# Performance work log

Measured on AMD Instinct MI355X. Metric: run time of the kernel, lower is better.

The kernel has to match this reference:

```python
import jax, jax.numpy as jnp
import numpy as np

N = 100000   # nodes
E = 1000000  # edges
IN = 100     # input feature dim
H = 4        # heads
D = 32       # hidden per head (H*D = 128)
C = 47       # classes
EPS = 1e-5
SLOPE = 0.2  # DGL GATv2 leaky_relu negative slope


def setup_inputs() -> dict:
    key = jax.random.key(0)
    ks = jax.random.split(key, 32)
    lin = lambda k, i, o: (jax.random.normal(k, (i, o), jnp.float32) / np.float32(np.sqrt(i)))
    inp = {}
    inp['x'] = jax.random.normal(ks[0], (N, IN), jnp.float32)
    inp['src'] = jax.random.randint(ks[1], (E,), 0, N, jnp.int32)
    inp['dst'] = jnp.sort(jax.random.randint(ks[2], (E,), 0, N, jnp.int32))
    # layer 0: IN -> H*D, Linear residual (IN != H*D)
    inp['Wsrc0'] = lin(ks[3], IN, H * D); inp['bsrc0'] = jnp.zeros(H * D, jnp.float32)
    inp['Wdst0'] = lin(ks[4], IN, H * D); inp['bdst0'] = jnp.zeros(H * D, jnp.float32)
    inp['attn0'] = lin(ks[5], H, D)
    inp['Wres0'] = lin(ks[6], IN, H * D); inp['bres0'] = jnp.zeros(H * D, jnp.float32)
    # layer 1: H*D -> H*D, Identity residual (128 == 128)
    inp['Wsrc1'] = lin(ks[7], H * D, H * D); inp['bsrc1'] = jnp.zeros(H * D, jnp.float32)
    inp['Wdst1'] = lin(ks[8], H * D, H * D); inp['bdst1'] = jnp.zeros(H * D, jnp.float32)
    inp['attn1'] = lin(ks[9], H, D)
    # layer 2: H*D -> H*C, Linear residual (128 != 188)
    inp['Wsrc2'] = lin(ks[10], H * D, H * C); inp['bsrc2'] = jnp.zeros(H * C, jnp.float32)
    inp['Wdst2'] = lin(ks[11], H * D, H * C); inp['bdst2'] = jnp.zeros(H * C, jnp.float32)
    inp['attn2'] = lin(ks[12], H, C)
    inp['Wres2'] = lin(ks[13], H * D, H * C); inp['bres2'] = jnp.zeros(H * C, jnp.float32)
    # BatchNorm1d params (training-mode batch stats)
    inp['g0'] = jnp.ones(H * D, jnp.float32); inp['be0'] = jnp.zeros(H * D, jnp.float32)
    inp['g1'] = jnp.ones(H * D, jnp.float32); inp['be1'] = jnp.zeros(H * D, jnp.float32)
    return inp


def _gatv2(h, src, dst, Ws, bs, Wd, bd, attn, resval):
    """One GATv2Conv on a full block (src feats == dst feats == h)."""
    Hh, Dd = attn.shape
    fs = (h @ Ws + bs).reshape(-1, Hh, Dd)   # [N,H,D] src projection
    fd = (h @ Wd + bd).reshape(-1, Hh, Dd)   # [N,H,D] dst projection
    e = jax.nn.leaky_relu(fs[src] + fd[dst], SLOPE)         # [E,H,D]
    logits = jnp.einsum('ehd,hd->eh', e, attn)              # [E,H]
    m = jax.ops.segment_max(logits, dst, num_segments=N)    # per-dst max
    ex = jnp.exp(logits - m[dst])
    s = jax.ops.segment_sum(ex, dst, num_segments=N)
    alpha = ex / s[dst]                                      # edge softmax
    out = jax.ops.segment_sum(alpha[:, :, None] * fs[src], dst, num_segments=N)
    return out + resval                                      # [N,H,D]


def _bn(x, g, b):
    mu = x.mean(0)
    v = x.var(0)  # biased, as torch BN training mode
    return g * (x - mu) / jnp.sqrt(v + EPS) + b


def reference(x, src, dst,
              Wsrc0, bsrc0, Wdst0, bdst0, attn0, Wres0, bres0,
              Wsrc1, bsrc1, Wdst1, bdst1, attn1,
              Wsrc2, bsrc2, Wdst2, bdst2, attn2, Wres2, bres2,
              g0, be0, g1, be1):
    # layer 0: conv(+relu activation) -> flatten -> BN -> relu (dropout = eval identity)
    res0 = (x @ Wres0 + bres0).reshape(N, H, D)
    h = jax.nn.relu(_gatv2(x, src, dst, Wsrc0, bsrc0, Wdst0, bdst0, attn0, res0))
    h = jax.nn.relu(_bn(h.reshape(N, H * D), g0, be0))
    # layer 1: Identity residual
    res1 = h.reshape(N, H, D)
    h = jax.nn.relu(_gatv2(h, src, dst, Wsrc1, bsrc1, Wdst1, bdst1, attn1, res1))
    h = jax.nn.relu(_bn(h.reshape(N, H * D), g1, be1))
    # layer 2: no activation; mean over heads; log_softmax
    res2 = (h @ Wres2 + bres2).reshape(N, H, C)
    h = _gatv2(h, src, dst, Wsrc2, bsrc2, Wdst2, bdst2, attn2, res2)
    h = h.mean(1)                                # [N,C]
    return jax.nn.log_softmax(h, axis=-1)
```

## Files before the change

kernel.cpp:

```cpp
#include <hip/hip_runtime.h>
#include <hip/hip_bf16.h>

#define Nn 100000
#define Ee 1000000
#define INF_ 100
#define Hh 4
#define Dd 32
#define HD 128
#define Cc 47
#define HC 188
#define HCP 192
#define EPSV 1e-5f
#define SLOPE 0.2f
#define NBLK ((Nn + 255) / 256)

typedef __hip_bfloat16 bf16;
typedef __attribute__((ext_vector_type(8))) short short8;
typedef __attribute__((ext_vector_type(4))) float f32x4;
typedef __attribute__((ext_vector_type(2))) float f32x2;

__device__ __forceinline__ float tof(bf16 v) { return __bfloat162float(v); }
__device__ __forceinline__ float b2f(unsigned short u) {
    return __uint_as_float((unsigned)u << 16);
}
__device__ __forceinline__ float b2flo(unsigned u) {
    return __uint_as_float(u << 16);
}
__device__ __forceinline__ float b2fhi(unsigned u) {
    return __uint_as_float(u & 0xFFFF0000u);
}
__device__ __forceinline__ float ldb(const bf16* p) {
    return b2f(*(const unsigned short*)p);
}
__device__ __forceinline__ unsigned short f2u(float v) {
    bf16 t = __float2bfloat16(v);
    return *(unsigned short*)&t;
}
__device__ __forceinline__ f32x2 pk2(float x, float y) {
    f32x2 r; r.x = x; r.y = y; return r;
}
__device__ __forceinline__ f32x2 pabs2(f32x2 v) {
    return __builtin_elementwise_max(v, -v);
}
__device__ __forceinline__ f32x2 pfma2(f32x2 a, f32x2 b, f32x2 c) {
    return __builtin_elementwise_fma(a, b, c);
}

template <int C>
__device__ __forceinline__ float dppadd(float v) {
    int m = __builtin_amdgcn_update_dpp(0, __float_as_int(v), C, 0xF, 0xF, false);
    return v + __int_as_float(m);
}
template <int C>
__device__ __forceinline__ float dppmax(float v) {
    int m = __builtin_amdgcn_update_dpp(0, __float_as_int(v), C, 0xF, 0xF, false);
    return fmaxf(v, __int_as_float(m));
}
__device__ __forceinline__ float sum16(float p) {
    p = dppadd<0xB1>(p);
    p = dppadd<0x4E>(p);
    p = dppadd<0x124>(p);
    p = dppadd<0x128>(p);
    return p;
}
__device__ __forceinline__ float max16(float p) {
    p = dppmax<0xB1>(p); p = dppmax<0x4E>(p);
    p = dppmax<0x124>(p); p = dppmax<0x128>(p);
    return p;
}

#define L2E 1.4426950408889634f
#define LN2 0.6931471805599453f

__global__ void detect_dtype(const unsigned* __restrict__ x, int* __restrict__ flag) {
    if (blockIdx.x == 0 && threadIdx.x == 0) {
        int good = 0;
        for (int i = 0; i < 256; ++i) {
            unsigned lo = x[i] & 0xFFFFu;
            float v = __uint_as_float(lo << 16);
            float a = fabsf(v);
            if (a > 1e-4f && a < 10.f) good++;
        }
        *flag = (good >= 128) ? 1 : 0;
    }
}

__device__ __forceinline__ float ld_any(const void* p, int i, int isbf) {
    return isbf ? tof(((const bf16*)p)[i]) : ((const float*)p)[i];
}

__global__ void cvt_x(const void* __restrict__ in, bf16* __restrict__ out,
                      const int* __restrict__ flag) {
    int i = blockIdx.x * blockDim.x + threadIdx.x;
    if (i >= Nn * 128) return;
    int row = i >> 7, col = i & 127;
    float v = (col < INF_) ? ld_any(in, row * INF_ + col, *flag) : 0.f;
    out[i] = __float2bfloat16(v);
}

#define NSP 15
struct CvtTab { const void* src[NSP]; int off[NSP + 1]; };

__global__ void cvt_params(CvtTab t, bf16* __restrict__ out, int total,
                           const int* __restrict__ flag) {
    int i = blockIdx.x * blockDim.x + threadIdx.x;
    if (i >= total) return;
    int isbf = *flag;
    int seg = 0;
    while (i >= t.off[seg + 1]) seg++;
    out[i] = __float2bfloat16(ld_any(t.src[seg], i - t.off[seg], isbf));
}

#define WROWS 1280
struct PrepTab { const void* src[8]; int row0[8]; int K[8]; int M[8]; int MP[8]; };

__global__ void prep_all(PrepTab t, bf16* __restrict__ wtb, const int* __restrict__ flag) {
    int i = blockIdx.x * blockDim.x + threadIdx.x;
    if (i >= WROWS * 128) return;
    int row = i >> 7, k = i & 127;
    int isbf = *flag;
    float v = 0.f;
#pragma unroll
    for (int q = 0; q < 8; ++q) {
        if (row >= t.row0[q] && row < t.row0[q] + t.MP[q]) {
            int m = row - t.row0[q];
            if (m < t.M[q] && k < t.K[q])
                v = ld_any(t.src[q], k * t.M[q] + m, isbf);
        }
    }
    wtb[i] = __float2bfloat16(v);
}

__global__ void zero_u32(unsigned* __restrict__ p, int n) {
    int i = blockIdx.x * blockDim.x + threadIdx.x;
    if (i < n) p[i] = 0u;
}

__global__ void src_scale_ptr(const int* __restrict__ src, const int* __restrict__ dst,
                              unsigned* __restrict__ w384, unsigned* __restrict__ w256,
                              int* __restrict__ ptr) {
    int i = blockIdx.x * blockDim.x + threadIdx.x;
    if (i < Ee) {
        unsigned s = (unsigned)src[i];
        w384[i] = s * 384u;
        w256[i] = s << 8;
    }
    if (i <= Nn) {
        if (i == Nn) { ptr[Nn] = Ee; return; }
        int lo = 0, hi = Ee;
        while (lo < hi) {
            int mid = (lo + hi) >> 1;
            if (dst[mid] < i) lo = mid + 1; else hi = mid;
        }
        ptr[i] = lo;
    }
}

__global__ void deg_hist_blk(const int* __restrict__ ptr, int* __restrict__ cnt) {
    __shared__ int lh[256];
    int t = threadIdx.x;
    lh[t] = 0;
    __syncthreads();
    int n = blockIdx.x * 256 + t;
    if (n < Nn) {
        int dg = ptr[n + 1] - ptr[n]; if (dg > 255) dg = 255;
        atomicAdd(&lh[dg], 1);
    }
    __syncthreads();
    cnt[t * NBLK + blockIdx.x] = lh[t];
}

__global__ void deg_totals(const int* __restrict__ cnt, int* __restrict__ totals) {
    int wave = threadIdx.x >> 6, lane = threadIdx.x & 63;
    int bin = blockIdx.x * 4 + wave;
    int s = 0;
    for (int k = lane; k < NBLK; k += 64) s += cnt[bin * NBLK + k];
#pragma unroll
    for (int o = 1; o < 64; o <<= 1) s += __shfl_xor(s, o);
    if (lane == 0) totals[bin] = s;
}

__global__ void deg_bases(const int* __restrict__ cnt, const int* __restrict__ totals,
                          int* __restrict__ base) {
    int wave = threadIdx.x >> 6, lane = threadIdx.x & 63;
    int bin = blockIdx.x * 4 + wave;
    int bb = 0;
    for (int b = bin + 1 + lane; b < 256; b += 64) bb += totals[b];
#pragma unroll
    for (int o = 1; o < 64; o <<= 1) bb += __shfl_xor(bb, o);
    int run = bb;
    for (int k0 = 0; k0 < NBLK; k0 += 64) {
        int k = k0 + lane;
        int c = (k < NBLK) ? cnt[bin * NBLK + k] : 0;
        int p = c;
#pragma unroll
        for (int o = 1; o < 64; o <<= 1) {
            int t = __shfl_up(p, o);
            if (lane >= o) p += t;
        }
        if (k < NBLK) base[bin * NBLK + k] = run + (p - c);
        run += __shfl(p, 63);
    }
}

__global__ void deg_scatter_blk(const int* __restrict__ ptr, const int* __restrict__ base,
                                int* __restrict__ perm) {
    __shared__ int lh[256];
    int t = threadIdx.x;
    lh[t] = 0;
    __syncthreads();
    int n = blockIdx.x * 256 + t;
    if (n < Nn) {
        int dg = ptr[n + 1] - ptr[n]; if (dg > 255) dg = 255;
        int loc = atomicAdd(&lh[dg], 1);
        perm[base[dg * NBLK + blockIdx.x] + loc] = n;
    }
}

template <int MP, int NOUT, int CS, bool ABN, bool PACK, int OSTR, int NY>
__global__ __launch_bounds__(256, 4) void gemm_big(
    const bf16* __restrict__ A, const bf16* __restrict__ Wt,
    const bf16* __restrict__ b0, const bf16* __restrict__ b1,
    const bf16* __restrict__ b2,
    bf16* __restrict__ o0, bf16* __restrict__ o1, bf16* __restrict__ o2,
    int MR, const float* __restrict__ bnp) {
    __shared__ __align__(16) bf16 Al[64 * 136];
    const int row0 = blockIdx.x * 64;
    const int tid = threadIdx.x;
#pragma unroll
    for (int j = 0; j < 4; ++j) {
        int idx = tid + j * 256;
        int r = idx >> 4, kk = (idx & 15) * 8;
        int4 val = {0, 0, 0, 0};
        if (row0 + r < Nn) {
            val = *(const int4*)&A[(size_t)(row0 + r) * 128 + kk];
            if (ABN) {
                short8 av = *(short8*)&val;
                bf16 tmp[8];
#pragma unroll
                for (int u = 0; u < 8; ++u) {
                    float v = b2f((unsigned short)av[u]);
                    v = fmaxf(fmaf(v, bnp[kk + u], bnp[128 + kk + u]), 0.f);
                    tmp[u] = __float2bfloat16(v);
                }
                val = *(int4*)tmp;
            }
        }
        *(int4*)&Al[r * 136 + kk] = val;
    }
    __syncthreads();
    const int wave = tid >> 6, lane = tid & 63;
    const int n16 = lane & 15, quad = lane >> 4;
    const bf16* ap = Al + n16 * 136 + quad * 8;
#pragma unroll
    for (int ny = 0; ny < NY; ++ny) {
        const int colbase = ny * (64 * CS) + wave * (16 * CS);
        f32x4 acc[4][CS];
#pragma unroll
        for (int rt = 0; rt < 4; ++rt)
#pragma unroll
            for (int c = 0; c < CS; ++c) acc[rt][c] = (f32x4){0.f, 0.f, 0.f, 0.f};
        const bf16* wb[CS];
#pragma unroll
        for (int c = 0; c < CS; ++c)
            wb[c] = Wt + (size_t)(colbase + c * 16 + n16) * 128 + quad * 8;
#pragma unroll
        for (int ks = 0; ks < 4; ++ks) {
            short8 bf[CS];
#pragma unroll
            for (int c = 0; c < CS; ++c) bf[c] = *(const short8*)(wb[c] + ks * 32);
#pragma unroll
            for (int rt = 0; rt < 4; ++rt) {
                short8 af = *(const short8*)(ap + rt * 16 * 136 + ks * 32);
#pragma unroll
                for (int c = 0; c < CS; ++c)
                    acc[rt][c] = __builtin_amdgcn_mfma_f32_16x16x32_bf16(af, bf[c], acc[rt][c], 0, 0, 0);
            }
        }
#pragma unroll
        for (int c = 0; c < CS; ++c) {
            int col = colbase + c * 16 + n16;
            int oi = col / MP, lc = col - oi * MP;
            if (oi >= NOUT || lc >= MR) continue;
            const bf16* bp = (oi == 0) ? b0 : (oi == 1) ? b1 : b2;
            bf16* o = (oi == 0) ? o0 : (oi == 1) ? o1 : o2;
            float bb = tof(bp[lc]);
            int st;
            if (PACK) {
                int hh = lc / 47, cc = lc - hh * 47;
                int jj = cc & 15, kk2 = cc >> 4;
                int l = hh * 16 + jj;
                st = (kk2 < 2) ? (2 * l + kk2) : (128 + l);
            } else {
                st = lc;
            }
#pragma unroll
            for (int rt = 0; rt < 4; ++rt) {
#pragma unroll
                for (int i = 0; i < 4; ++i) {
                    int row = row0 + rt * 16 + quad * 4 + i;
                    if (row < Nn)
                        o[(size_t)row * OSTR + st] = __float2bfloat16(acc[rt][c][i] + bb);
                }
            }
        }
    }
}

template <bool RESBN>
__global__ __launch_bounds__(256) void gat_fused_128(
    const bf16* __restrict__ fs, const bf16* __restrict__ fd,
    const unsigned* __restrict__ srcW, const int* __restrict__ ptr,
    const int* __restrict__ perm,
    const bf16* __restrict__ attn, const bf16* __restrict__ resb,
    const float* __restrict__ bnp, bf16* __restrict__ hout) {
    const int wave = threadIdx.x >> 6, lane = threadIdx.x & 63;
    const int di = blockIdx.x * 4 + wave;
    if (di >= Nn) return;
    const int d = perm[di];
    const int c0 = lane * 2;
    const unsigned c0b = (unsigned)c0 * 2u;
    ushort2 aq = *(const ushort2*)&attn[c0];
    float a0 = b2f(aq.x) * L2E, a1 = b2f(aq.y) * L2E;
    const f32x2 Av = pk2(0.6f * a0, 0.6f * a1);
    const f32x2 Bv = pk2(0.4f * a0, 0.4f * a1);
    ushort2 dq = *(const ushort2*)&fd[(size_t)d * HD + c0];
    const f32x2 fdv = pk2(b2f(dq.x), b2f(dq.y));
    const char* fsb = (const char*)fs;
    float l = 0.f;
    f32x2 Ov = pk2(0.f, 0.f);
    int e = ptr[d];
    const int e1 = ptr[d + 1];
    for (; e < e1 && (e & 3); ++e) {
        unsigned v = srcW[e] + c0b;
        ushort2 fq = *(const ushort2*)(fsb + v);
        f32x2 f = pk2(b2f(fq.x), b2f(fq.y));
        f32x2 x = f + fdv;
        f32x2 t = pfma2(pabs2(x), Bv, x * Av);
        float p = sum16(t.x + t.y);
        float pe = __builtin_amdgcn_exp2f(p);
        l += pe;
        Ov = pfma2(pk2(pe, pe), f, Ov);
    }
    for (; e + 3 < e1; e += 4) {
        uint4 sw = *(const uint4*)&srcW[e];
        unsigned vA = sw.x + c0b, vB = sw.y + c0b;
        unsigned vC = sw.z + c0b, vD = sw.w + c0b;
        ushort2 qA = *(const ushort2*)(fsb + vA);
        ushort2 qB = *(const ushort2*)(fsb + vB);
        ushort2 qC = *(const ushort2*)(fsb + vC);
        ushort2 qD = *(const ushort2*)(fsb + vD);
        f32x2 fA = pk2(b2f(qA.x), b2f(qA.y));
        f32x2 fB = pk2(b2f(qB.x), b2f(qB.y));
        f32x2 fC = pk2(b2f(qC.x), b2f(qC.y));
        f32x2 fD = pk2(b2f(qD.x), b2f(qD.y));
        f32x2 xA = fA + fdv, xB = fB + fdv, xC = fC + fdv, xD = fD + fdv;
        f32x2 tA = pfma2(pabs2(xA), Bv, xA * Av);
        f32x2 tB = pfma2(pabs2(xB), Bv, xB * Av);
        f32x2 tC = pfma2(pabs2(xC), Bv, xC * Av);
        f32x2 tD = pfma2(pabs2(xD), Bv, xD * Av);
        float pA = tA.x + tA.y, pB = tB.x + tB.y;
        float pC = tC.x + tC.y, pD = tD.x + tD.y;
        pA = sum16(pA); pB = sum16(pB); pC = sum16(pC); pD = sum16(pD);
        float eA = __builtin_amdgcn_exp2f(pA), eB = __builtin_amdgcn_exp2f(pB);
        float eC = __builtin_amdgcn_exp2f(pC), eD = __builtin_amdgcn_exp2f(pD);
        l += (eA + eB) + (eC + eD);
        Ov = pfma2(pk2(eA, eA), fA, Ov);
        Ov = pfma2(pk2(eB, eB), fB, Ov);
        Ov = pfma2(pk2(eC, eC), fC, Ov);
        Ov = pfma2(pk2(eD, eD), fD, Ov);
    }
    for (; e < e1; ++e) {
        unsigned v = srcW[e] + c0b;
        ushort2 fq = *(const ushort2*)(fsb + v);
        f32x2 f = pk2(b2f(fq.x), b2f(fq.y));
        f32x2 x = f + fdv;
        f32x2 t = pfma2(pabs2(x), Bv, x * Av);
        float p = sum16(t.x + t.y);
        float pe = __builtin_amdgcn_exp2f(p);
        l += pe;
        Ov = pfma2(pk2(pe, pe), f, Ov);
    }
    float inv = l > 0.f ? 1.f / l : 0.f;
    ushort2 rq = *(const ushort2*)&resb[(size_t)d * HD + c0];
    float r0 = b2f(rq.x), r1 = b2f(rq.y);
    if (RESBN) {
        r0 = fmaxf(fmaf(r0, bnp[c0], bnp[HD + c0]), 0.f);
        r1 = fmaxf(fmaf(r1, bnp[c0 + 1], bnp[HD + c0 + 1]), 0.f);
    }
    float v0 = fmaxf(fmaf(Ov.x, inv, r0), 0.f);
    float v1 = fmaxf(fmaf(Ov.y, inv, r1), 0.f);
    ushort2 ov; ov.x = f2u(v0); ov.y = f2u(v1);
    *(ushort2*)&hout[(size_t)d * HD + c0] = ov;
}

__global__ __launch_bounds__(256) void gat_fused_188(
    const bf16* __restrict__ fs, const bf16* __restrict__ fd,
    const unsigned* __restrict__ srcW, const int* __restrict__ ptr,
    const int* __restrict__ perm,
    const bf16* __restrict__ attn, const bf16* __restrict__ rs,
    void* __restrict__ out, const int* __restrict__ flag) {
    const int wave = threadIdx.x >> 6, lane = threadIdx.x & 63;
    const int di = blockIdx.x * 4 + wave;
    if (di >= Nn) return;
    const int d = perm[di];
    const int h = lane >> 4, j = lane & 15;
    const unsigned cbA = (unsigned)lane * 4u;
    const unsigned cbB = 256u + (unsigned)lane * 2u;
    const int ca = h * Cc + j;
    const bool has2 = (j < 15);
    float a0 = ldb(&attn[ca]) * L2E;
    float a1 = ldb(&attn[ca + 16]) * L2E;
    float a2 = has2 ? ldb(&attn[ca + 32]) * L2E : 0.f;
    const f32x2 Av = pk2(0.6f * a0, 0.6f * a1);
    const f32x2 Bv = pk2(0.4f * a0, 0.4f * a1);
    const float A2 = 0.6f * a2, B2 = 0.4f * a2;
    const char* fdb = (const char*)fd;
    const size_t drow = (size_t)d * 384u;
    unsigned dqa = *(const unsigned*)(fdb + drow + cbA);
    unsigned short dqb = *(const unsigned short*)(fdb + drow + cbB);
    const f32x2 fdv = pk2(b2flo(dqa), b2fhi(dqa));
    const float fd2 = b2f(dqb);
    const char* fsb = (const char*)fs;
    float l = 0.f, O2 = 0.f;
    f32x2 Ov = pk2(0.f, 0.f);
    int e = ptr[d];
    const int e1 = ptr[d + 1];
    for (; e < e1 && (e & 3); ++e) {
        unsigned b = srcW[e];
        unsigned q = *(const unsigned*)(fsb + b + cbA);
        unsigned short u = *(const unsigned short*)(fsb + b + cbB);
        f32x2 f = pk2(b2flo(q), b2fhi(q)); float g = b2f(u);
        f32x2 x = f + fdv;
        float y = g + fd2;
        f32x2 t = pfma2(pabs2(x), Bv, x * Av);
        float p = fmaf(y, A2, fmaf(fabsf(y), B2, t.x + t.y));
        p = sum16(p);
        float pe = __builtin_amdgcn_exp2f(p);
        l += pe;
        Ov = pfma2(pk2(pe, pe), f, Ov); O2 = fmaf(pe, g, O2);
    }
    for (; e + 3 < e1; e += 4) {
        uint4 sw = *(const uint4*)&srcW[e];
        unsigned bA = sw.x, bB = sw.y, bC = sw.z, bD = sw.w;
        unsigned qA = *(const unsigned*)(fsb + bA + cbA);
        unsigned qB = *(const unsigned*)(fsb + bB + cbA);
        unsigned qC = *(const unsigned*)(fsb + bC + cbA);
        unsigned qD = *(const unsigned*)(fsb + bD + cbA);
        unsigned short uA = *(const unsigned short*)(fsb + bA + cbB);
        unsigned short uB = *(const unsigned short*)(fsb + bB + cbB);
        unsigned short uC = *(const unsigned short*)(fsb + bC + cbB);
        unsigned short uD = *(const unsigned short*)(fsb + bD + cbB);
        f32x2 fA = pk2(b2flo(qA), b2fhi(qA)); float gA = b2f(uA);
        f32x2 fB = pk2(b2flo(qB), b2fhi(qB)); float gB = b2f(uB);
        f32x2 fC = pk2(b2flo(qC), b2fhi(qC)); float gC = b2f(uC);
        f32x2 fD = pk2(b2flo(qD), b2fhi(qD)); float gD = b2f(uD);
        f32x2 xA = fA + fdv, xB = fB + fdv, xC = fC + fdv, xD = fD + fdv;
        float yA = gA + fd2, yB = gB + fd2, yC = gC + fd2, yD = gD + fd2;
        f32x2 tA = pfma2(pabs2(xA), Bv, xA * Av);
        f32x2 tB = pfma2(pabs2(xB), Bv, xB * Av);
        f32x2 tC = pfma2(pabs2(xC), Bv, xC * Av);
        f32x2 tD = pfma2(pabs2(xD), Bv, xD * Av);
        float pA = fmaf(yA, A2, fmaf(fabsf(yA), B2, tA.x + tA.y));
        float pB = fmaf(yB, A2, fmaf(fabsf(yB), B2, tB.x + tB.y));
        float pC = fmaf(yC, A2, fmaf(fabsf(yC), B2, tC.x + tC.y));
        float pD = fmaf(yD, A2, fmaf(fabsf(yD), B2, tD.x + tD.y));
        pA = sum16(pA); pB = sum16(pB); pC = sum16(pC); pD = sum16(pD);
        float eA = __builtin_amdgcn_exp2f(pA), eB = __builtin_amdgcn_exp2f(pB);
        float eC = __builtin_amdgcn_exp2f(pC), eD = __builtin_amdgcn_exp2f(pD);
        l += (eA + eB) + (eC + eD);
        Ov = pfma2(pk2(eA, eA), fA, Ov); O2 = fmaf(eA, gA, O2);
        Ov = pfma2(pk2(eB, eB), fB, Ov); O2 = fmaf(eB, gB, O2);
        Ov = pfma2(pk2(eC, eC), fC, Ov); O2 = fmaf(eC, gC, O2);
        Ov = pfma2(pk2(eD, eD), fD, Ov); O2 = fmaf(eD, gD, O2);
    }
    for (; e < e1; ++e) {
        unsigned b = srcW[e];
        unsigned q = *(const unsigned*)(fsb + b + cbA);
        unsigned short u = *(const unsigned short*)(fsb + b + cbB);
        f32x2 f = pk2(b2flo(q), b2fhi(q)); float g = b2f(u);
        f32x2 x = f + fdv;
        float y = g + fd2;
        f32x2 t = pfma2(pabs2(x), Bv, x * Av);
        float p = fmaf(y, A2, fmaf(fabsf(y), B2, t.x + t.y));
        p = sum16(p);
        float pe = __builtin_amdgcn_exp2f(p);
        l += pe;
        Ov = pfma2(pk2(pe, pe), f, Ov); O2 = fmaf(pe, g, O2);
    }
    float inv = l > 0.f ? 1.f / l : 0.f;
    const char* rb_ = (const char*)rs;
    unsigned rqa = *(const unsigned*)(rb_ + drow + cbA);
    unsigned short rqb = *(const unsigned short*)(rb_ + drow + cbB);
    float v0 = fmaf(Ov.x, inv, b2flo(rqa));
    float v1 = fmaf(Ov.y, inv, b2fhi(rqa));
    float v2 = has2 ? fmaf(O2, inv, b2f(rqb)) : 0.f;
    v0 += __shfl_xor(v0, 16); v0 += __shfl_xor(v0, 32); v0 *= 0.25f;
    v1 += __shfl_xor(v1, 16); v1 += __shfl_xor(v1, 32); v1 *= 0.25f;
    v2 += __shfl_xor(v2, 16); v2 += __shfl_xor(v2, 32); v2 *= 0.25f;
    float mx = fmaxf(v0, v1);
    if (has2) mx = fmaxf(mx, v2);
    mx = max16(mx);
    float sm = __expf(v0 - mx) + __expf(v1 - mx) + (has2 ? __expf(v2 - mx) : 0.f);
    sm = sum16(sm);
    if (h == 0) {
        float ls = mx + __log2f(sm) * LN2;
        if (*flag) {
            bf16* o = (bf16*)out + (size_t)d * Cc;
            o[j] = __float2bfloat16(v0 - ls);
            o[j + 16] = __float2bfloat16(v1 - ls);
            if (has2) o[j + 32] = __float2bfloat16(v2 - ls);
        } else {
            float* o = (float*)out + (size_t)d * Cc;
            o[j] = v0 - ls;
            o[j + 16] = v1 - ls;
            if (has2) o[j + 32] = v2 - ls;
        }
    }
}

__global__ void col_stats(const bf16* __restrict__ in, float* __restrict__ sums) {
    int c = threadIdx.x;
    int r0 = blockIdx.x * 256;
    int r1 = r0 + 256; if (r1 > Nn) r1 = Nn;
    float s = 0.f, s2 = 0.f;
    for (int r = r0; r < r1; ++r) {
        float v = ldb(&in[(size_t)r * HD + c]);
        s += v; s2 += v * v;
    }
    atomicAdd(&sums[c], s);
    atomicAdd(&sums[HD + c], s2);
}

__global__ void bn_finalize(const float* __restrict__ sums, const bf16* __restrict__ g,
                            const bf16* __restrict__ be, float* __restrict__ ss) {
    int c = threadIdx.x;
    float mu = sums[c] * (1.f / Nn);
    float var = sums[HD + c] * (1.f / Nn) - mu * mu;
    float sc = tof(g[c]) * rsqrtf(var + EPSV);
    ss[c] = sc;
    ss[HD + c] = tof(be[c]) - mu * sc;
}

extern "C" void kernel_launch(void* const* d_in, const int* in_sizes, int n_in,
                              void* d_out, int out_size, void* d_ws, size_t ws_size,
                              hipStream_t stream) {
    (void)in_sizes; (void)n_in; (void)out_size; (void)ws_size;
    const void* x = d_in[0];
    const int* src = (const int*)d_in[1];
    const int* dst = (const int*)d_in[2];

    char* ws = (char*)d_ws;
    size_t off = 0;
    auto alloc = [&](size_t bytes) {
        void* p = ws + off;
        off += (bytes + 255) & ~(size_t)255;
        return p;
    };
    bf16* xb = (bf16*)alloc((size_t)Nn * 128 * 2);
    bf16* rb = (bf16*)alloc((size_t)Nn * HD * 2);
    bf16* rs = xb;
    bf16* fs = (bf16*)alloc((size_t)Nn * HCP * 2);
    bf16* fd = (bf16*)alloc((size_t)Nn * HCP * 2);
    bf16* hbA = (bf16*)alloc((size_t)Nn * HD * 2);
    bf16* hbB = (bf16*)alloc((size_t)Nn * HD * 2);
    int* ptr = (int*)alloc((Nn + 1) * 4);
    bf16* wtb = (bf16*)alloc((size_t)WROWS * 128 * 2);
    float* bns = (float*)alloc(2 * HD * 4);
    float* bnss0 = (float*)alloc(2 * HD * 4);
    float* bnss1 = (float*)alloc(2 * HD * 4);
    bf16* pb = (bf16*)alloc(4096 * 2);
    int* flag = (int*)alloc(256);
    unsigned* w384 = (unsigned*)alloc((size_t)Ee * 4);
    unsigned* w256 = (unsigned*)alloc((size_t)Ee * 4);
    int* cnt = (int*)alloc((size_t)256 * NBLK * 4);
    int* cbase = (int*)alloc((size_t)256 * NBLK * 4);
    int* totals = (int*)alloc(256 * 4);
    int* perm = (int*)alloc((size_t)Nn * 4);

    static const int spIdx[NSP] = {4, 6, 7, 9, 11, 13, 14, 16, 18, 19, 21, 22, 23, 24, 25};
    static const int spSz[NSP]  = {HD, HD, HD, HD, HD, HD, HD, HC, HC, HC, HC, HD, HD, HD, HD};
    CvtTab tab;
    int tot = 0;
    for (int i = 0; i < NSP; ++i) { tab.src[i] = d_in[spIdx[i]]; tab.off[i] = tot; tot += spSz[i]; }
    tab.off[NSP] = tot;
    const bf16 *bsrc0 = pb + tab.off[0], *bdst0 = pb + tab.off[1], *attn0 = pb + tab.off[2],
               *bres0 = pb + tab.off[3], *bsrc1 = pb + tab.off[4], *bdst1 = pb + tab.off[5],
               *attn1 = pb + tab.off[6], *bsrc2 = pb + tab.off[7], *bdst2 = pb + tab.off[8],
               *attn2 = pb + tab.off[9], *bres2 = pb + tab.off[10],
               *g0 = pb + tab.off[11], *be0 = pb + tab.off[12],
               *g1 = pb + tab.off[13], *be1 = pb + tab.off[14];

    PrepTab pt;
    static const int wIdx[8] = {3, 5, 8, 10, 12, 15, 17, 20};
    static const int wK[8]   = {INF_, INF_, INF_, HD, HD, HD, HD, HD};
    static const int wM[8]   = {HD, HD, HD, HD, HD, HC, HC, HC};
    static const int wMP[8]  = {128, 128, 128, 128, 128, 192, 192, 192};
    static const int wR0[8]  = {0, 128, 256, 384, 512, 640, 832, 1024};
    for (int i = 0; i < 8; ++i) {
        pt.src[i] = d_in[wIdx[i]]; pt.row0[i] = wR0[i];
        pt.K[i] = wK[i]; pt.M[i] = wM[i]; pt.MP[i] = wMP[i];
    }

    detect_dtype<<<1, 64, 0, stream>>>((const unsigned*)x, flag);
    cvt_x<<<(Nn * 128 + 255) / 256, 256, 0, stream>>>(x, xb, flag);
    cvt_params<<<(tot + 255) / 256, 256, 0, stream>>>(tab, pb, tot, flag);
    prep_all<<<(WROWS * 128 + 255) / 256, 256, 0, stream>>>(pt, wtb, flag);
    src_scale_ptr<<<(Ee + 255) / 256, 256, 0, stream>>>(src, dst, w384, w256, ptr);
    deg_hist_blk<<<NBLK, 256, 0, stream>>>(ptr, cnt);
    deg_totals<<<64, 256, 0, stream>>>(cnt, totals);
    deg_bases<<<64, 256, 0, stream>>>(cnt, totals, cbase);
    deg_scatter_blk<<<NBLK, 256, 0, stream>>>(ptr, cbase, perm);

    const int fusedGrid = (Nn + 3) / 4;
    const int statsGrid = NBLK;
    const int rowBlk = (Nn + 63) / 64;

    gemm_big<128, 3, 3, false, false, HD, 2><<<rowBlk, 256, 0, stream>>>(
        xb, wtb, bsrc0, bdst0, bres0, fs, fd, rb, HD, nullptr);
    gat_fused_128<false><<<fusedGrid, 256, 0, stream>>>(fs, fd, w256, ptr, perm,
                                                        attn0, rb, nullptr, hbA);
    zero_u32<<<1, 256, 0, stream>>>((unsigned*)bns, 2 * HD);
    col_stats<<<statsGrid, 128, 0, stream>>>(hbA, bns);
    bn_finalize<<<1, HD, 0, stream>>>(bns, g0, be0, bnss0);

    gemm_big<128, 2, 2, true, false, HD, 2><<<rowBlk, 256, 0, stream>>>(
        hbA, wtb + (size_t)384 * 128, bsrc1, bdst1, nullptr, fs, fd, nullptr, HD, bnss0);
    gat_fused_128<true><<<fusedGrid, 256, 0, stream>>>(fs, fd, w256, ptr, perm,
                                                       attn1, hbA, bnss0, hbB);
    zero_u32<<<1, 256, 0, stream>>>((unsigned*)bns, 2 * HD);
    col_stats<<<statsGrid, 128, 0, stream>>>(hbB, bns);
    bn_finalize<<<1, HD, 0, stream>>>(bns, g1, be1, bnss1);

    gemm_big<192, 3, 3, true, true, HCP, 3><<<rowBlk, 256, 0, stream>>>(
        hbB, wtb + (size_t)640 * 128, bsrc2, bdst2, bres2, fs, fd, rs, HC, bnss1);
    gat_fused_188<<<fusedGrid, 256, 0, stream>>>(fs, fd, w384, ptr, perm, attn2, rs,
                                                 d_out, flag);
}
```

Measured before the change: 704.8 us.

## Merge setup kernels, split GEMM column tiles across grid y, widen GAT blocks

Merges the parameter conversion into the weight-prep kernel and moves the BN-stat zeroing into src_scale_ptr, using separate stat buffers per layer so two zero_u32 launches go away. The GEMM column loop (NY) becomes a second grid dimension, giving more independent blocks at the cost of each block reloading its A tile into LDS. The GAT kernels go from 4 to 8 waves per block. Launch count drops and parallelism rises, but A-tile loads and LDS traffic are duplicated across the grid-y blocks.

Measured after the change: 698.3 us. About the same (-0.9%).

```diff
diff --git a/kernel.cpp b/kernel.cpp
--- a/kernel.cpp
+++ b/kernel.cpp
@@ -98,53 +98,47 @@
     out[i] = __float2bfloat16(v);
 }
 
+#define WROWS 1280
 #define NSP 15
+struct PrepTab { const void* src[8]; int row0[8]; int K[8]; int M[8]; int MP[8]; };
 struct CvtTab { const void* src[NSP]; int off[NSP + 1]; };
 
-__global__ void cvt_params(CvtTab t, bf16* __restrict__ out, int total,
-                           const int* __restrict__ flag) {
+__global__ void prep_all(PrepTab t, CvtTab ct, bf16* __restrict__ wtb,
+                         bf16* __restrict__ pb, int total,
+                         const int* __restrict__ flag) {
     int i = blockIdx.x * blockDim.x + threadIdx.x;
-    if (i >= total) return;
     int isbf = *flag;
-    int seg = 0;
-    while (i >= t.off[seg + 1]) seg++;
-    out[i] = __float2bfloat16(ld_any(t.src[seg], i - t.off[seg], isbf));
-}
-
-#define WROWS 1280
-struct PrepTab { const void* src[8]; int row0[8]; int K[8]; int M[8]; int MP[8]; };
-
-__global__ void prep_all(PrepTab t, bf16* __restrict__ wtb, const int* __restrict__ flag) {
-    int i = blockIdx.x * blockDim.x + threadIdx.x;
-    if (i >= WROWS * 128) return;
-    int row = i >> 7, k = i & 127;
-    int isbf = *flag;
-    float v = 0.f;
-#pragma unroll
-    for (int q = 0; q < 8; ++q) {
-        if (row >= t.row0[q] && row < t.row0[q] + t.MP[q]) {
-            int m = row - t.row0[q];
-            if (m < t.M[q] && k < t.K[q])
-                v = ld_any(t.src[q], k * t.M[q] + m, isbf);
-        }
-    }
-    wtb[i] = __float2bfloat16(v);
-}
-
-__global__ void zero_u32(unsigned* __restrict__ p, int n) {
-    int i = blockIdx.x * blockDim.x + threadIdx.x;
-    if (i < n) p[i] = 0u;
+    if (i < WROWS * 128) {
+        int row = i >> 7, k = i & 127;
+        float v = 0.f;
+#pragma unroll
+        for (int q = 0; q < 8; ++q) {
+            if (row >= t.row0[q] && row < t.row0[q] + t.MP[q]) {
+                int m = row - t.row0[q];
+                if (m < t.M[q] && k < t.K[q])
+                    v = ld_any(t.src[q], k * t.M[q] + m, isbf);
+            }
+        }
+        wtb[i] = __float2bfloat16(v);
+    }
+    if (i < total) {
+        int seg = 0;
+        while (i >= ct.off[seg + 1]) seg++;
+        pb[i] = __float2bfloat16(ld_any(ct.src[seg], i - ct.off[seg], isbf));
+    }
 }
 
 __global__ void src_scale_ptr(const int* __restrict__ src, const int* __restrict__ dst,
                               unsigned* __restrict__ w384, unsigned* __restrict__ w256,
-                              int* __restrict__ ptr) {
+                              int* __restrict__ ptr,
+                              float* __restrict__ z0, float* __restrict__ z1) {
     int i = blockIdx.x * blockDim.x + threadIdx.x;
     if (i < Ee) {
         unsigned s = (unsigned)src[i];
         w384[i] = s * 384u;
         w256[i] = s << 8;
     }
+    if (i < 2 * HD) { z0[i] = 0.f; z1[i] = 0.f; }
     if (i <= Nn) {
         if (i == Nn) { ptr[Nn] = Ee; return; }
         int lo = 0, hi = Ee;
@@ -217,7 +211,7 @@
     }
 }
 
-template <int MP, int NOUT, int CS, bool ABN, bool PACK, int OSTR, int NY>
+template <int MP, int NOUT, int CS, bool ABN, bool PACK, int OSTR>
 __global__ __launch_bounds__(256, 4) void gemm_big(
     const bf16* __restrict__ A, const bf16* __restrict__ Wt,
     const bf16* __restrict__ b0, const bf16* __restrict__ b1,
@@ -251,71 +245,68 @@
     __syncthreads();
     const int wave = tid >> 6, lane = tid & 63;
     const int n16 = lane & 15, quad = lane >> 4;
+    const int colbase = blockIdx.y * (64 * CS) + wave * (16 * CS);
+    f32x4 acc[4][CS];
+#pragma unroll
+    for (int rt = 0; rt < 4; ++rt)
+#pragma unroll
+        for (int c = 0; c < CS; ++c) acc[rt][c] = (f32x4){0.f, 0.f, 0.f, 0.f};
+    const bf16* wb[CS];
+#pragma unroll
+    for (int c = 0; c < CS; ++c)
+        wb[c] = Wt + (size_t)(colbase + c * 16 + n16) * 128 + quad * 8;
     const bf16* ap = Al + n16 * 136 + quad * 8;
 #pragma unroll
-    for (int ny = 0; ny < NY; ++ny) {
-        const int colbase = ny * (64 * CS) + wave * (16 * CS);
-        f32x4 acc[4][CS];
-#pragma unroll
-        for (int rt = 0; rt < 4; ++rt)
-#pragma unroll
-            for (int c = 0; c < CS; ++c) acc[rt][c] = (f32x4){0.f, 0.f, 0.f, 0.f};
-        const bf16* wb[CS];
-#pragma unroll
-        for (int c = 0; c < CS; ++c)
-            wb[c] = Wt + (size_t)(colbase + c * 16 + n16) * 128 + quad * 8;
-#pragma unroll
-        for (int ks = 0; ks < 4; ++ks) {
-            short8 bf[CS];
-#pragma unroll
-            for (int c = 0; c < CS; ++c) bf[c] = *(const short8*)(wb[c] + ks * 32);
-#pragma unroll
-            for (int rt = 0; rt < 4; ++rt) {
-                short8 af = *(const short8*)(ap + rt * 16 * 136 + ks * 32);
-#pragma unroll
-                for (int c = 0; c < CS; ++c)
-                    acc[rt][c] = __builtin_amdgcn_mfma_f32_16x16x32_bf16(af, bf[c], acc[rt][c], 0, 0, 0);
+    for (int ks = 0; ks < 4; ++ks) {
+        short8 bf[CS];
+#pragma unroll
+        for (int c = 0; c < CS; ++c) bf[c] = *(const short8*)(wb[c] + ks * 32);
+#pragma unroll
+        for (int rt = 0; rt < 4; ++rt) {
+            short8 af = *(const short8*)(ap + rt * 16 * 136 + ks * 32);
+#pragma unroll
+            for (int c = 0; c < CS; ++c)
+                acc[rt][c] = __builtin_amdgcn_mfma_f32_16x16x32_bf16(af, bf[c], acc[rt][c], 0, 0, 0);
+        }
+    }
+#pragma unroll
+    for (int c = 0; c < CS; ++c) {
+        int col = colbase + c * 16 + n16;
+        int oi = col / MP, lc = col - oi * MP;
+        if (oi >= NOUT || lc >= MR) continue;
+        const bf16* bp = (oi == 0) ? b0 : (oi == 1) ? b1 : b2;
+        bf16* o = (oi == 0) ? o0 : (oi == 1) ? o1 : o2;
+        float bb = tof(bp[lc]);
+        int st;
+        if (PACK) {
+            int hh = lc / 47, cc = lc - hh * 47;
+            int jj = cc & 15, kk2 = cc >> 4;
+            int l = hh * 16 + jj;
+            st = (kk2 < 2) ? (2 * l + kk2) : (128 + l);
+        } else {
+            st = lc;
+        }
+#pragma unroll
+        for (int rt = 0; rt < 4; ++rt) {
+#pragma unroll
+            for (int i = 0; i < 4; ++i) {
+                int row = row0 + rt * 16 + quad * 4 + i;
+                if (row < Nn)
+                    o[(size_t)row * OSTR + st] = __float2bfloat16(acc[rt][c][i] + bb);
             }
         }
-#pragma unroll
-        for (int c = 0; c < CS; ++c) {
-            int col = colbase + c * 16 + n16;
-            int oi = col / MP, lc = col - oi * MP;
-            if (oi >= NOUT || lc >= MR) continue;
-            const bf16* bp = (oi == 0) ? b0 : (oi == 1) ? b1 : b2;
-            bf16* o = (oi == 0) ? o0 : (oi == 1) ? o1 : o2;
-            float bb = tof(bp[lc]);
-            int st;
-            if (PACK) {
-                int hh = lc / 47, cc = lc - hh * 47;
-                int jj = cc & 15, kk2 = cc >> 4;
-                int l = hh * 16 + jj;
-                st = (kk2 < 2) ? (2 * l + kk2) : (128 + l);
-            } else {
-                st = lc;
-            }
-#pragma unroll
-            for (int rt = 0; rt < 4; ++rt) {
-#pragma unroll
-                for (int i = 0; i < 4; ++i) {
-                    int row = row0 + rt * 16 + quad * 4 + i;
-                    if (row < Nn)
-                        o[(size_t)row * OSTR + st] = __float2bfloat16(acc[rt][c][i] + bb);
-                }
-            }
-        }
     }
 }
 
 template <bool RESBN>
-__global__ __launch_bounds__(256) void gat_fused_128(
+__global__ __launch_bounds__(512) void gat_fused_128(
     const bf16* __restrict__ fs, const bf16* __restrict__ fd,
     const unsigned* __restrict__ srcW, const int* __restrict__ ptr,
     const int* __restrict__ perm,
     const bf16* __restrict__ attn, const bf16* __restrict__ resb,
     const float* __restrict__ bnp, bf16* __restrict__ hout) {
     const int wave = threadIdx.x >> 6, lane = threadIdx.x & 63;
-    const int di = blockIdx.x * 4 + wave;
+    const int di = blockIdx.x * 8 + wave;
     if (di >= Nn) return;
     const int d = perm[di];
     const int c0 = lane * 2;
@@ -394,14 +385,14 @@
     *(ushort2*)&hout[(size_t)d * HD + c0] = ov;
 }
 
-__global__ __launch_bounds__(256) void gat_fused_188(
+__global__ __launch_bounds__(512) void gat_fused_188(
     const bf16* __restrict__ fs, const bf16* __restrict__ fd,
     const unsigned* __restrict__ srcW, const int* __restrict__ ptr,
     const int* __restrict__ perm,
     const bf16* __restrict__ attn, const bf16* __restrict__ rs,
     void* __restrict__ out, const int* __restrict__ flag) {
     const int wave = threadIdx.x >> 6, lane = threadIdx.x & 63;
-    const int di = blockIdx.x * 4 + wave;
+    const int di = blockIdx.x * 8 + wave;
     if (di >= Nn) return;
     const int d = perm[di];
     const int h = lane >> 4, j = lane & 15;
@@ -566,7 +557,8 @@
     bf16* hbB = (bf16*)alloc((size_t)Nn * HD * 2);
     int* ptr = (int*)alloc((Nn + 1) * 4);
     bf16* wtb = (bf16*)alloc((size_t)WROWS * 128 * 2);
-    float* bns = (float*)alloc(2 * HD * 4);
+    float* bns0 = (float*)alloc(2 * HD * 4);
+    float* bns1 = (float*)alloc(2 * HD * 4);
     float* bnss0 = (float*)alloc(2 * HD * 4);
     float* bnss1 = (float*)alloc(2 * HD * 4);
     bf16* pb = (bf16*)alloc(4096 * 2);
@@ -604,36 +596,34 @@
 
     detect_dtype<<<1, 64, 0, stream>>>((const unsigned*)x, flag);
     cvt_x<<<(Nn * 128 + 255) / 256, 256, 0, stream>>>(x, xb, flag);
-    cvt_params<<<(tot + 255) / 256, 256, 0, stream>>>(tab, pb, tot, flag);
-    prep_all<<<(WROWS * 128 + 255) / 256, 256, 0, stream>>>(pt, wtb, flag);
-    src_scale_ptr<<<(Ee + 255) / 256, 256, 0, stream>>>(src, dst, w384, w256, ptr);
+    prep_all<<<(WROWS * 128 + 255) / 256, 256, 0, stream>>>(pt, tab, wtb, pb, tot, flag);
+    src_scale_ptr<<<(Ee + 255) / 256, 256, 0, stream>>>(src, dst, w384, w256, ptr,
+                                                        bns0, bns1);
     deg_hist_blk<<<NBLK, 256, 0, stream>>>(ptr, cnt);
     deg_totals<<<64, 256, 0, stream>>>(cnt, totals);
     deg_bases<<<64, 256, 0, stream>>>(cnt, totals, cbase);
     deg_scatter_blk<<<NBLK, 256, 0, stream>>>(ptr, cbase, perm);
 
-    const int fusedGrid = (Nn + 3) / 4;
+    const int fusedGrid = (Nn + 7) / 8;
     const int statsGrid = NBLK;
     const int rowBlk = (Nn + 63) / 64;
 
-    gemm_big<128, 3, 3, false, false, HD, 2><<<rowBlk, 256, 0, stream>>>(
+    gemm_big<128, 3, 3, false, false, HD><<<dim3(rowBlk, 2), 256, 0, stream>>>(
         xb, wtb, bsrc0, bdst0, bres0, fs, fd, rb, HD, nullptr);
-    gat_fused_128<false><<<fusedGrid, 256, 0, stream>>>(fs, fd, w256, ptr, perm,
+    gat_fused_128<false><<<fusedGrid, 512, 0, stream>>>(fs, fd, w256, ptr, perm,
                                                         attn0, rb, nullptr, hbA);
-    zero_u32<<<1, 256, 0, stream>>>((unsigned*)bns, 2 * HD);
-    col_stats<<<statsGrid, 128, 0, stream>>>(hbA, bns);
-    bn_finalize<<<1, HD, 0, stream>>>(bns, g0, be0, bnss0);
-
-    gemm_big<128, 2, 2, true, false, HD, 2><<<rowBlk, 256, 0, stream>>>(
+    col_stats<<<statsGrid, 128, 0, stream>>>(hbA, bns0);
+    bn_finalize<<<1, HD, 0, stream>>>(bns0, g0, be0, bnss0);
+
+    gemm_big<128, 2, 2, true, false, HD><<<dim3(rowBlk, 2), 256, 0, stream>>>(
         hbA, wtb + (size_t)384 * 128, bsrc1, bdst1, nullptr, fs, fd, nullptr, HD, bnss0);
-    gat_fused_128<true><<<fusedGrid, 256, 0, stream>>>(fs, fd, w256, ptr, perm,
+    gat_fused_128<true><<<fusedGrid, 512, 0, stream>>>(fs, fd, w256, ptr, perm,
                                                        attn1, hbA, bnss0, hbB);
-    zero_u32<<<1, 256, 0, stream>>>((unsigned*)bns, 2 * HD);
-    col_stats<<<statsGrid, 128, 0, stream>>>(hbB, bns);
-    bn_finalize<<<1, HD, 0, stream>>>(bns, g1, be1, bnss1);
-
-    gemm_big<192, 3, 3, true, true, HCP, 3><<<rowBlk, 256, 0, stream>>>(
+    col_stats<<<statsGrid, 128, 0, stream>>>(hbB, bns1);
+    bn_finalize<<<1, HD, 0, stream>>>(bns1, g1, be1, bnss1);
+
+    gemm_big<192, 3, 3, true, true, HCP><<<dim3(rowBlk, 3), 256, 0, stream>>>(
         hbB, wtb + (size_t)640 * 128, bsrc2, bdst2, bres2, fs, fd, rs, HC, bnss1);
-    gat_fused_188<<<fusedGrid, 256, 0, stream>>>(fs, fd, w384, ptr, perm, attn2, rs,
+    gat_fused_188<<<fusedGrid, 512, 0, stream>>>(fs, fd, w384, ptr, perm, attn2, rs,
                                                  d_out, flag);
 }
```
